# Optimization experiments

Hardware: AMD Instinct MI355X
Metric: run time of the kernel (lower is better)

The kernel has to match this reference:

```python
import jax, jax.numpy as jnp
import numpy as np
from jax import lax

K = 3          # kernel_size
OUT = 256      # out_channels
IN_CPG = 256   # in_channels // groups
GROUPS = 1
STRIDE = 1
PAD = 1
DN = ('NCHW', 'OIHW', 'NCHW')


def _bounds(i, n, o):
    return int(np.floor(i * n / o)), int(np.ceil((i + 1) * n / o))


def adaptive_pool2d(x, o, reduce_fn):
    # Faithful torch AdaptiveAvg/MaxPool2d: static bin boundaries.
    H, W = x.shape[2], x.shape[3]
    rows = []
    for i in range(o):
        r0, r1 = _bounds(i, H, o)
        cells = []
        for j in range(o):
            c0, c1 = _bounds(j, W, o)
            cells.append(reduce_fn(x[:, :, r0:r1, c0:c1], axis=(2, 3)))
        rows.append(jnp.stack(cells, axis=-1))
    return jnp.stack(rows, axis=-2)  # (B, C, o, o)


def _gconv(x, w, fg, pad='VALID'):
    return lax.conv_general_dilated(x, w, (1, 1), pad,
                                    dimension_numbers=DN,
                                    feature_group_count=fg)


def setup_inputs() -> dict:
    key = jax.random.key(0)
    ks = jax.random.split(key, 7)
    s = 0.05
    return {
        'x':     jax.random.normal(ks[0], (32, 256, 56, 56), jnp.float32),
        'w1':    jax.random.normal(ks[1], (IN_CPG, GROUPS, 3, 3), jnp.float32) * s,
        'b1':    jax.random.normal(ks[2], (IN_CPG,), jnp.float32) * s,
        'w2':    jax.random.normal(ks[3], (OUT * IN_CPG, 1, 1, 1), jnp.float32) * s,
        'b2':    jax.random.normal(ks[4], (OUT * IN_CPG,), jnp.float32) * s,
        'w_att': jax.random.normal(ks[5], (OUT * IN_CPG, GROUPS, 3, 3), jnp.float32) * s,
        'b_att': jax.random.normal(ks[6], (OUT * IN_CPG,), jnp.float32) * s,
    }


def reference(x, w1, b1, w2, b2, w_att, b_att):
    B, C, H, W = x.shape
    # attention branch: maxpool -> grouped 3x3 conv -> sigmoid
    maxi = adaptive_pool2d(x, K + 2, jnp.max)                    # (B, C, K+2, K+2)
    att = _gconv(maxi, w_att, IN_CPG) + b_att[None, :, None, None]  # (B, OUT*IN_CPG, K, K)
    att = jax.nn.sigmoid(att).reshape(B * OUT, IN_CPG, K, K)
    # weight branch: avgpool -> depthwise 3x3 -> relu -> grouped 1x1
    avg = adaptive_pool2d(x, K + 2, jnp.mean)                    # (B, C, K+2, K+2)
    wgt = jax.nn.relu(_gconv(avg, w1, IN_CPG) + b1[None, :, None, None])  # (B, IN_CPG, K, K)
    wgt = _gconv(wgt, w2, IN_CPG) + b2[None, :, None, None]      # (B, OUT*IN_CPG, K, K)
    wgt = wgt.reshape(B * OUT, IN_CPG, K, K)
    # per-sample dynamic conv as grouped conv with batch-as-groups
    xg = x.reshape(1, B * C, H, W)
    out = lax.conv_general_dilated(xg, wgt * att, (STRIDE, STRIDE),
                                   [(PAD, PAD), (PAD, PAD)],
                                   dimension_numbers=DN,
                                   feature_group_count=GROUPS * B)
    return out.reshape(B, OUT, out.shape[-2], out.shape[-1])
```

## Files before the change

### kernel.cpp

```cpp
#include <hip/hip_runtime.h>
#include <hip/hip_bf16.h>

#define BATCH 32
#define CIN   256
#define OCH   256
#define HW    56
#define PW    58
#define PAREA (PW*PW)
#define PLANE (HW*HW)

typedef float float4v __attribute__((ext_vector_type(4)));
typedef short short8  __attribute__((ext_vector_type(8)));

__device__ __forceinline__ unsigned short f2bf(float f) {
  union { float f; unsigned u; } v; v.f = f;
  unsigned r = v.u + 0x7fffu + ((v.u >> 16) & 1u);
  return (unsigned short)(r >> 16);
}

__global__ __launch_bounds__(256) void pool_kernel(const float* __restrict__ x,
                                                   float* __restrict__ avgp,
                                                   float* __restrict__ maxp) {
  __shared__ float plane[PLANE];
  int bc = blockIdx.x;
  const float* src = x + (size_t)bc * PLANE;
  for (int e = threadIdx.x; e < PLANE; e += 256) plane[e] = src[e];
  __syncthreads();
  if (threadIdx.x < 25) {
    int i = threadIdx.x / 5, j = threadIdx.x % 5;
    int r0 = (i * HW) / 5, r1 = ((i + 1) * HW + 4) / 5;
    int c0 = (j * HW) / 5, c1 = ((j + 1) * HW + 4) / 5;
    float s = 0.f, m = -1e30f;
    for (int r = r0; r < r1; ++r)
      for (int c = c0; c < c1; ++c) {
        float v = plane[r * HW + c];
        s += v; m = fmaxf(m, v);
      }
    avgp[(size_t)bc * 25 + threadIdx.x] = s / (float)((r1 - r0) * (c1 - c0));
    maxp[(size_t)bc * 25 + threadIdx.x] = m;
  }
}

__global__ __launch_bounds__(256) void wcalc_kernel(
    const float* __restrict__ avgp, const float* __restrict__ maxp,
    const float* __restrict__ w1, const float* __restrict__ b1,
    const float* __restrict__ w2, const float* __restrict__ b2,
    const float* __restrict__ watt, const float* __restrict__ batt,
    unsigned short* __restrict__ Wbf) {
  int blk = blockIdx.x;
  int oc = blk & 255, b = blk >> 8;
  __shared__ float s_avg[25], s_max[25], s_w1[9], s_wgt1[9];
  int tid = threadIdx.x;
  size_t base = ((size_t)b * 256 + oc) * 25;
  if (tid < 25) { s_avg[tid] = avgp[base + tid]; s_max[tid] = maxp[base + tid]; }
  if (tid >= 32 && tid < 41) s_w1[tid - 32] = w1[oc * 9 + (tid - 32)];
  __syncthreads();
  if (tid < 9) {
    int ky = tid / 3, kx = tid % 3;
    float acc = b1[oc];
    for (int u = 0; u < 3; ++u)
      for (int v = 0; v < 3; ++v)
        acc += s_avg[(ky + u) * 5 + kx + v] * s_w1[u * 3 + v];
    s_wgt1[tid] = fmaxf(acc, 0.f);
  }
  __syncthreads();
  int ic = tid;
  size_t g = (size_t)oc * 256 + ic;
  float wa[9];
#pragma unroll
  for (int r = 0; r < 9; ++r) wa[r] = watt[g * 9 + r];
  float ba = batt[g], w2v = w2[g], b2v = b2[g];
#pragma unroll
  for (int r = 0; r < 9; ++r) {
    int ky = r / 3, kx = r % 3;
    float s = ba;
#pragma unroll
    for (int u = 0; u < 3; ++u)
#pragma unroll
      for (int v = 0; v < 3; ++v)
        s += s_max[(ky + u) * 5 + kx + v] * wa[u * 3 + v];
    float att = 1.f / (1.f + __expf(-s));
    float wv = (s_wgt1[r] * w2v + b2v) * att;
    Wbf[(((size_t)b * 9 + r) * 256 + oc) * 256 + ic] = f2bf(wv);
  }
}

__global__ __launch_bounds__(256) void border_kernel(unsigned short* __restrict__ xp) {
  int bid = blockIdx.x;
  int b = bid / 228, bi = bid % 228;
  int pos;
  if (bi < 58)       pos = bi;
  else if (bi < 116) pos = 57 * PW + (bi - 58);
  else if (bi < 172) pos = (bi - 116 + 1) * PW;
  else               pos = (bi - 172 + 1) * PW + 57;
  xp[((size_t)b * PAREA + pos) * 256 + threadIdx.x] = 0;
}

__global__ __launch_bounds__(256) void xprep_kernel(const float* __restrict__ x,
                                                    unsigned short* __restrict__ xp) {
  int bid = blockIdx.x;
  int y = bid % 56; int t2 = bid / 56; int icb = t2 & 3; int b = t2 >> 2;
  __shared__ float tr[56][65];
  for (int e = threadIdx.x; e < 56 * 64; e += 256) {
    int icl = e / 56, col = e % 56;
    tr[col][icl] = x[((size_t)(b * 256 + icb * 64 + icl)) * PLANE + y * HW + col];
  }
  __syncthreads();
  for (int e = threadIdx.x; e < 448; e += 256) {
    int col = e >> 3, c8 = e & 7;
    short8 v;
#pragma unroll
    for (int k = 0; k < 8; ++k) v[k] = (short)f2bf(tr[col][c8 * 8 + k]);
    size_t dst = ((size_t)b * PAREA + (size_t)(y + 1) * PW + (col + 1)) * 256 + icb * 64 + c8 * 8;
    *(short8*)&xp[dst] = v;
  }
}

__global__ __launch_bounds__(256, 2) void conv_kernel(
    const unsigned short* __restrict__ xp,
    const unsigned short* __restrict__ Wbf,
    float* __restrict__ out) {
  __shared__ unsigned short bpl[348 * 32];
  __shared__ unsigned short apl[128 * 32];

  int bid = blockIdx.x;
  int rt = bid % 14; int t2 = bid / 14; int ocb = t2 & 1; int b = t2 >> 1;
  int y0 = rt * 4;
  int tid = threadIdx.x;
  int lane = tid & 63, w = tid >> 6;
  int mw = w & 1, nw = w >> 1;
  int quad = lane >> 4, l16 = lane & 15;

  int basepos[7];
#pragma unroll
  for (int nt = 0; nt < 7; ++nt) {
    int n = nw * 112 + nt * 16 + l16;
    basepos[nt] = (n / 56) * PW + (n % 56);
  }

  float4v acc[4][7];
#pragma unroll
  for (int mt = 0; mt < 4; ++mt)
#pragma unroll
    for (int nt = 0; nt < 7; ++nt)
      acc[mt][nt] = (float4v){0.f, 0.f, 0.f, 0.f};

  const size_t xbase = ((size_t)b * PAREA + (size_t)y0 * PW) * 256;

  for (int icb = 0; icb < 8; ++icb) {
    __syncthreads();
    for (int e = tid; e < 1392; e += 256) {
      int c = e & 3, p = e >> 2;
      *(short8*)&bpl[p * 32 + c * 8] =
          *(const short8*)&xp[xbase + (size_t)p * 256 + icb * 32 + c * 8];
    }
    for (int r = 0; r < 9; ++r) {
      __syncthreads();
      const size_t wbase = (((size_t)b * 9 + r) * 256 + ocb * 128) * 256 + icb * 32;
      for (int e = tid; e < 512; e += 256) {
        int c = e & 3, oc = e >> 2;
        *(short8*)&apl[oc * 32 + c * 8] =
            *(const short8*)&Wbf[wbase + (size_t)oc * 256 + c * 8];
      }
      __syncthreads();
      int ky = r / 3, kx = r - ky * 3;
      int poff = (ky * PW + kx) * 32;
      short8 bfrag[7];
#pragma unroll
      for (int nt = 0; nt < 7; ++nt)
        bfrag[nt] = *(const short8*)&bpl[basepos[nt] * 32 + poff + quad * 8];
#pragma unroll
      for (int mt = 0; mt < 4; ++mt) {
        short8 afrag = *(const short8*)&apl[(mw * 64 + mt * 16 + l16) * 32 + quad * 8];
#pragma unroll
        for (int nt = 0; nt < 7; ++nt)
          acc[mt][nt] = __builtin_amdgcn_mfma_f32_16x16x32_bf16(afrag, bfrag[nt], acc[mt][nt], 0, 0, 0);
      }
    }
  }

#pragma unroll
  for (int mt = 0; mt < 4; ++mt) {
    int m = ocb * 128 + mw * 64 + mt * 16 + quad * 4;
#pragma unroll
    for (int nt = 0; nt < 7; ++nt) {
      int n = nw * 112 + nt * 16 + l16;
      int yy = y0 + n / 56, xx = n % 56;
      size_t o = (((size_t)b * 256 + m) * 56 + yy) * 56 + xx;
#pragma unroll
      for (int reg = 0; reg < 4; ++reg)
        out[o + (size_t)reg * PLANE] = acc[mt][nt][reg];
    }
  }
}

extern "C" void kernel_launch(void* const* d_in, const int* in_sizes, int n_in,
                              void* d_out, int out_size, void* d_ws, size_t ws_size,
                              hipStream_t stream) {
  const float* x    = (const float*)d_in[0];
  const float* w1   = (const float*)d_in[1];
  const float* b1   = (const float*)d_in[2];
  const float* w2   = (const float*)d_in[3];
  const float* b2   = (const float*)d_in[4];
  const float* watt = (const float*)d_in[5];
  const float* batt = (const float*)d_in[6];
  float* out = (float*)d_out;

  float* avgp = (float*)d_ws;
  float* maxp = avgp + 204800;
  unsigned short* Wbf = (unsigned short*)(maxp + 204800);
  unsigned short* xp  = Wbf + (size_t)32 * 9 * 256 * 256;

  pool_kernel<<<BATCH * CIN, 256, 0, stream>>>(x, avgp, maxp);
  wcalc_kernel<<<BATCH * OCH, 256, 0, stream>>>(avgp, maxp, w1, b1, w2, b2, watt, batt, Wbf);
  border_kernel<<<BATCH * 228, 256, 0, stream>>>(xp);
  xprep_kernel<<<BATCH * 4 * 56, 256, 0, stream>>>(x, xp);
  conv_kernel<<<BATCH * 2 * 14, 256, 0, stream>>>(xp, Wbf, out);
}
```

Measured before the change: 464.3 us.

## Fuse pooling into weight calc, async LDS loads and double-buffer conv weights

Merges the pooling and weight-generation kernels into one kernel, which removes an intermediate buffer and a launch. Pooling becomes a separable column-then-row reduction. The conv kernel now uses global_load_lds direct-to-LDS copies with a 64-channel K step, a re-laid-out LDS tile and a double-buffered weight tile, so the next tap's weights load during the MFMAs. Block order is remapped so that blocks sharing a row tile run together. xprep uses float4 reads. The cost is more LDS use and more complex sync.

```diff
diff --git a/kernel.cpp b/kernel.cpp
--- a/kernel.cpp
+++ b/kernel.cpp
@@ -2,8 +2,6 @@
 #include <hip/hip_bf16.h>
 
 #define BATCH 32
-#define CIN   256
-#define OCH   256
 #define HW    56
 #define PW    58
 #define PAREA (PW*PW)
@@ -18,42 +16,51 @@
   return (unsigned short)(r >> 16);
 }
 
-__global__ __launch_bounds__(256) void pool_kernel(const float* __restrict__ x,
-                                                   float* __restrict__ avgp,
-                                                   float* __restrict__ maxp) {
-  __shared__ float plane[PLANE];
-  int bc = blockIdx.x;
-  const float* src = x + (size_t)bc * PLANE;
-  for (int e = threadIdx.x; e < PLANE; e += 256) plane[e] = src[e];
-  __syncthreads();
-  if (threadIdx.x < 25) {
-    int i = threadIdx.x / 5, j = threadIdx.x % 5;
-    int r0 = (i * HW) / 5, r1 = ((i + 1) * HW + 4) / 5;
-    int c0 = (j * HW) / 5, c1 = ((j + 1) * HW + 4) / 5;
-    float s = 0.f, m = -1e30f;
-    for (int r = r0; r < r1; ++r)
-      for (int c = c0; c < c1; ++c) {
-        float v = plane[r * HW + c];
-        s += v; m = fmaxf(m, v);
-      }
-    avgp[(size_t)bc * 25 + threadIdx.x] = s / (float)((r1 - r0) * (c1 - c0));
-    maxp[(size_t)bc * 25 + threadIdx.x] = m;
-  }
-}
-
-__global__ __launch_bounds__(256) void wcalc_kernel(
-    const float* __restrict__ avgp, const float* __restrict__ maxp,
+__device__ __forceinline__ void gl_lds16(const unsigned short* g, unsigned short* l) {
+  __builtin_amdgcn_global_load_lds(
+      (const __attribute__((address_space(1))) unsigned int*)(const void*)g,
+      (__attribute__((address_space(3))) unsigned int*)(void*)l, 16, 0, 0);
+}
+
+__global__ __launch_bounds__(256) void poolw_kernel(
+    const float* __restrict__ x,
     const float* __restrict__ w1, const float* __restrict__ b1,
     const float* __restrict__ w2, const float* __restrict__ b2,
     const float* __restrict__ watt, const float* __restrict__ batt,
     unsigned short* __restrict__ Wbf) {
+  __shared__ float plane[PLANE];
+  __shared__ float colS[5 * 56], colM[5 * 56];
+  __shared__ float s_avg[25], s_max[25], s_w1[9], s_wgt1[9];
   int blk = blockIdx.x;
   int oc = blk & 255, b = blk >> 8;
-  __shared__ float s_avg[25], s_max[25], s_w1[9], s_wgt1[9];
   int tid = threadIdx.x;
-  size_t base = ((size_t)b * 256 + oc) * 25;
-  if (tid < 25) { s_avg[tid] = avgp[base + tid]; s_max[tid] = maxp[base + tid]; }
+  const float* src = x + (size_t)(b * 256 + oc) * PLANE;
+  for (int e = tid; e < PLANE; e += 256) plane[e] = src[e];
   if (tid >= 32 && tid < 41) s_w1[tid - 32] = w1[oc * 9 + (tid - 32)];
+  __syncthreads();
+  for (int e = tid; e < 280; e += 256) {
+    int j = e / 56, r = e - j * 56;
+    int c0 = (j * 56) / 5, c1 = ((j + 1) * 56 + 4) / 5;
+    float s = 0.f, m = -1e30f;
+    for (int c = c0; c < c1; ++c) {
+      float v = plane[r * 56 + c];
+      s += v; m = fmaxf(m, v);
+    }
+    colS[j * 56 + r] = s; colM[j * 56 + r] = m;
+  }
+  __syncthreads();
+  if (tid < 25) {
+    int i = tid / 5, j = tid - i * 5;
+    int r0 = (i * 56) / 5, r1 = ((i + 1) * 56 + 4) / 5;
+    int c0 = (j * 56) / 5, c1 = ((j + 1) * 56 + 4) / 5;
+    float s = 0.f, m = -1e30f;
+    for (int r = r0; r < r1; ++r) {
+      s += colS[j * 56 + r];
+      m = fmaxf(m, colM[j * 56 + r]);
+    }
+    s_avg[tid] = s / (float)((r1 - r0) * (c1 - c0));
+    s_max[tid] = m;
+  }
   __syncthreads();
   if (tid < 9) {
     int ky = tid / 3, kx = tid % 3;
@@ -101,9 +108,14 @@
   int bid = blockIdx.x;
   int y = bid % 56; int t2 = bid / 56; int icb = t2 & 3; int b = t2 >> 2;
   __shared__ float tr[56][65];
-  for (int e = threadIdx.x; e < 56 * 64; e += 256) {
-    int icl = e / 56, col = e % 56;
-    tr[col][icl] = x[((size_t)(b * 256 + icb * 64 + icl)) * PLANE + y * HW + col];
+  for (int e = threadIdx.x; e < 64 * 14; e += 256) {
+    int icl = e / 14, q = e - icl * 14;
+    const float* sp = x + ((size_t)(b * 256 + icb * 64 + icl)) * PLANE + y * HW + q * 4;
+    float4 v = *(const float4*)sp;
+    tr[q * 4 + 0][icl] = v.x;
+    tr[q * 4 + 1][icl] = v.y;
+    tr[q * 4 + 2][icl] = v.z;
+    tr[q * 4 + 3][icl] = v.w;
   }
   __syncthreads();
   for (int e = threadIdx.x; e < 448; e += 256) {
@@ -120,11 +132,12 @@
     const unsigned short* __restrict__ xp,
     const unsigned short* __restrict__ Wbf,
     float* __restrict__ out) {
-  __shared__ unsigned short bpl[348 * 32];
-  __shared__ unsigned short apl[128 * 32];
+  __shared__ __align__(16) unsigned short bpl[8 * 348 * 8];
+  __shared__ __align__(16) unsigned short apl[2][8 * 128 * 8];
 
   int bid = blockIdx.x;
-  int rt = bid % 14; int t2 = bid / 14; int ocb = t2 & 1; int b = t2 >> 1;
+  int g = bid & 63, rt = bid >> 6;
+  int b = g >> 1, ocb = g & 1;
   int y0 = rt * 4;
   int tid = threadIdx.x;
   int lane = tid & 63, w = tid >> 6;
@@ -137,6 +150,9 @@
     int n = nw * 112 + nt * 16 + l16;
     basepos[nt] = (n / 56) * PW + (n % 56);
   }
+  int mrow[4];
+#pragma unroll
+  for (int mt = 0; mt < 4; ++mt) mrow[mt] = mw * 64 + mt * 16 + l16;
 
   float4v acc[4][7];
 #pragma unroll
@@ -147,35 +163,63 @@
 
   const size_t xbase = ((size_t)b * PAREA + (size_t)y0 * PW) * 256;
 
-  for (int icb = 0; icb < 8; ++icb) {
+  for (int icb = 0; icb < 4; ++icb) {
     __syncthreads();
-    for (int e = tid; e < 1392; e += 256) {
-      int c = e & 3, p = e >> 2;
-      *(short8*)&bpl[p * 32 + c * 8] =
-          *(const short8*)&xp[xbase + (size_t)p * 256 + icb * 32 + c * 8];
-    }
+    {
+      const unsigned short* xsrc = xp + xbase + (size_t)icb * 64;
+#pragma unroll
+      for (int it = 0; it < 11; ++it) {
+        int el = it * 64 + lane;
+        int cc = (el >= 348) ? 1 : 0;
+        int c = 2 * w + cc;
+        int p = el - cc * 348;
+        unsigned short* ldst = &bpl[((size_t)w * 696 + it * 64) * 8];
+        if (el < 696)
+          gl_lds16(xsrc + (size_t)p * 256 + c * 8, ldst);
+      }
+    }
+    {
+      size_t wb = (((size_t)b * 9 + 0) * 256 + ocb * 128) * 256 + (size_t)icb * 64;
+#pragma unroll
+      for (int it = 0; it < 4; ++it) {
+        int e = w * 256 + it * 64 + lane;
+        int c = e >> 7, oc = e & 127;
+        unsigned short* ldst = &apl[0][((size_t)w * 256 + it * 64) * 8];
+        gl_lds16(Wbf + wb + (size_t)oc * 256 + c * 8, ldst);
+      }
+    }
+    __syncthreads();
+
     for (int r = 0; r < 9; ++r) {
+      int buf = r & 1;
+      if (r < 8) {
+        size_t wb = (((size_t)b * 9 + (r + 1)) * 256 + ocb * 128) * 256 + (size_t)icb * 64;
+#pragma unroll
+        for (int it = 0; it < 4; ++it) {
+          int e = w * 256 + it * 64 + lane;
+          int c = e >> 7, oc = e & 127;
+          unsigned short* ldst = &apl[buf ^ 1][((size_t)w * 256 + it * 64) * 8];
+          gl_lds16(Wbf + wb + (size_t)oc * 256 + c * 8, ldst);
+        }
+      }
+      int ky = r / 3, kx = r - ky * 3;
+      int dpos = ky * PW + kx;
+#pragma unroll
+      for (int h = 0; h < 2; ++h) {
+        int hq = h * 4 + quad;
+        short8 bfrag[7];
+#pragma unroll
+        for (int nt = 0; nt < 7; ++nt)
+          bfrag[nt] = *(const short8*)&bpl[((size_t)hq * 348 + basepos[nt] + dpos) * 8];
+#pragma unroll
+        for (int mt = 0; mt < 4; ++mt) {
+          short8 afrag = *(const short8*)&apl[buf][((size_t)hq * 128 + mrow[mt]) * 8];
+#pragma unroll
+          for (int nt = 0; nt < 7; ++nt)
+            acc[mt][nt] = __builtin_amdgcn_mfma_f32_16x16x32_bf16(afrag, bfrag[nt], acc[mt][nt], 0, 0, 0);
+        }
+      }
       __syncthreads();
-      const size_t wbase = (((size_t)b * 9 + r) * 256 + ocb * 128) * 256 + icb * 32;
-      for (int e = tid; e < 512; e += 256) {
-        int c = e & 3, oc = e >> 2;
-        *(short8*)&apl[oc * 32 + c * 8] =
-            *(const short8*)&Wbf[wbase + (size_t)oc * 256 + c * 8];
-      }
-      __syncthreads();
-      int ky = r / 3, kx = r - ky * 3;
-      int poff = (ky * PW + kx) * 32;
-      short8 bfrag[7];
-#pragma unroll
-      for (int nt = 0; nt < 7; ++nt)
-        bfrag[nt] = *(const short8*)&bpl[basepos[nt] * 32 + poff + quad * 8];
-#pragma unroll
-      for (int mt = 0; mt < 4; ++mt) {
-        short8 afrag = *(const short8*)&apl[(mw * 64 + mt * 16 + l16) * 32 + quad * 8];
-#pragma unroll
-        for (int nt = 0; nt < 7; ++nt)
-          acc[mt][nt] = __builtin_amdgcn_mfma_f32_16x16x32_bf16(afrag, bfrag[nt], acc[mt][nt], 0, 0, 0);
-      }
     }
   }
 
@@ -206,14 +250,11 @@
   const float* batt = (const float*)d_in[6];
   float* out = (float*)d_out;
 
-  float* avgp = (float*)d_ws;
-  float* maxp = avgp + 204800;
-  unsigned short* Wbf = (unsigned short*)(maxp + 204800);
+  unsigned short* Wbf = (unsigned short*)d_ws;
   unsigned short* xp  = Wbf + (size_t)32 * 9 * 256 * 256;
 
-  pool_kernel<<<BATCH * CIN, 256, 0, stream>>>(x, avgp, maxp);
-  wcalc_kernel<<<BATCH * OCH, 256, 0, stream>>>(avgp, maxp, w1, b1, w2, b2, watt, batt, Wbf);
+  poolw_kernel<<<BATCH * 256, 256, 0, stream>>>(x, w1, b1, w2, b2, watt, batt, Wbf);
   border_kernel<<<BATCH * 228, 256, 0, stream>>>(xp);
   xprep_kernel<<<BATCH * 4 * 56, 256, 0, stream>>>(x, xp);
-  conv_kernel<<<BATCH * 2 * 14, 256, 0, stream>>>(xp, Wbf, out);
-}
+  conv_kernel<<<64 * 14, 256, 0, stream>>>(xp, Wbf, out);
+}
```

Measured after the change: 477.4 us. 2.8% more time.
